# Optimization experiments

Hardware: AMD Instinct MI355X
Metric: run time of the kernel (lower is better)

The kernel has to match this reference:

```python
import jax, jax.numpy as jnp
import numpy as np

B, S, HIDDEN = 2, 2048, 2048
HEADS, GROUPS, KVC = 16, 4, 128
HPG = HEADS // GROUPS  # heads per group
LAYER_INDEX = 2
SOFTMAX_SCALE = KVC ** -0.5
ROPE_THETA = 10000.0


def _rope_tables(seq_len, dim, dtype=jnp.float32):
    inv_freq = 1.0 / (ROPE_THETA ** (jnp.arange(0, dim, 2, dtype=jnp.float32) / dim))
    t = jnp.arange(seq_len, dtype=jnp.float32)
    freqs = jnp.outer(t, inv_freq)  # [S, dim/2]
    return jnp.cos(freqs).astype(dtype), jnp.sin(freqs).astype(dtype)


def _apply_rope(x, cos, sin):
    # x: [b, s, h, d]; rotate-half (GPT-NeoX style)
    d2 = x.shape[-1] // 2
    x1, x2 = x[..., :d2], x[..., d2:]
    c = cos[None, :, None, :]
    s = sin[None, :, None, :]
    return jnp.concatenate([x1 * c - x2 * s, x2 * c + x1 * s], axis=-1)


def setup_inputs() -> dict:
    key = jax.random.key(0)
    k1, k2, k3, k4 = jax.random.split(key, 4)
    std = HIDDEN ** -0.5
    return {
        "x": jax.random.normal(k1, (B, S, HIDDEN), dtype=jnp.float32),
        "w_q": jax.random.normal(k2, (HIDDEN, HEADS * KVC), dtype=jnp.float32) * std,
        "w_kv": jax.random.normal(k3, (HIDDEN, 2 * GROUPS * KVC), dtype=jnp.float32) * std,
        "w_dense": jax.random.normal(k4, (HEADS * KVC, HIDDEN), dtype=jnp.float32) * std,
    }


def reference(x, w_q, w_kv, w_dense):
    b, s, _ = x.shape
    # QKV projections
    q = (x @ w_q).reshape(b, s, HEADS, KVC)                 # [b,s,H,d]
    kv = (x @ w_kv).reshape(b, s, 2, GROUPS, KVC)
    k, v = kv[:, :, 0], kv[:, :, 1]                          # [b,s,G,d]
    # Rotary embeddings on q and k
    cos, sin = _rope_tables(s, KVC, x.dtype)
    q = _apply_rope(q, cos, sin)
    k = _apply_rope(k, cos, sin)
    # GQA attention with per-layer scaling trick:
    # scores computed at scale/softmax of layer_index, cast fp32, rescaled back.
    qg = q.reshape(b, s, GROUPS, HPG, KVC)
    scores = jnp.einsum("bqghd,bkgd->bghqk", qg, k) * (SOFTMAX_SCALE / LAYER_INDEX)
    scores = scores.astype(jnp.float32) * LAYER_INDEX
    # causal mask
    causal = jnp.tril(jnp.ones((s, s), dtype=bool))
    mask_value = jnp.finfo(jnp.float32).min
    scores = jnp.where(causal[None, None, None, :, :], scores, mask_value)
    probs = jax.nn.softmax(scores, axis=-1).astype(x.dtype)  # dropout p=0 (eval)
    ctx = jnp.einsum("bghqk,bkgd->bqghd", probs, v).reshape(b, s, HEADS * KVC)
    return ctx @ w_dense
```

## Files before the change

### kernel.cpp

```cpp
#include <hip/hip_runtime.h>
#include <hip/hip_bf16.h>
#include <stdint.h>

typedef unsigned short u16;
typedef __bf16 bf16x8 __attribute__((ext_vector_type(8)));
typedef float f32x4 __attribute__((ext_vector_type(4)));

#define S_LEN 2048
#define BATCH 2
#define NHEADS 16
#define NGROUPS 4
#define DHEAD 128
#define QKV_W 3072

__device__ __forceinline__ float bf2f(u16 u) {
  union { uint32_t i; float f; } v; v.i = ((uint32_t)u) << 16; return v.f;
}
__device__ __forceinline__ u16 f2bf(float f) {
  union { float f; uint32_t i; } v; v.f = f;
  uint32_t r = v.i + 0x7FFF + ((v.i >> 16) & 1);
  return (u16)(r >> 16);
}
__device__ __forceinline__ void llds16(const void* g, void* l) {
  __builtin_amdgcn_global_load_lds(
      (const __attribute__((address_space(1))) uint32_t*)g,
      (__attribute__((address_space(3))) uint32_t*)l, 16, 0, 0);
}

__device__ __forceinline__ void store_out(u16* C, long i, float v) { C[i] = f2bf(v); }
__device__ __forceinline__ void store_out(float* C, long i, float v) { C[i] = v; }

__global__ void rope_tables_k(float* __restrict__ cosT, float* __restrict__ sinT) {
  int i = blockIdx.x * 256 + threadIdx.x;
  int s = i >> 6, j = i & 63;
  float inv = exp2f(-(float)j * 0.20762050593045983f);
  float ang = (float)s * inv;
  float sv, cv;
  sincosf(ang, &sv, &cv);
  cosT[i] = cv; sinT[i] = sv;
}

__global__ void cvt_f32_bf16(const float* __restrict__ in, u16* __restrict__ out) {
  long i = ((long)blockIdx.x * 256 + threadIdx.x) * 4;
  float4 v = *(const float4*)(in + i);
  ushort4 o;
  o.x = f2bf(v.x); o.y = f2bf(v.y); o.z = f2bf(v.z); o.w = f2bf(v.w);
  *(ushort4*)(out + i) = o;
}

__global__ void transpose_f32_bf16(const float* __restrict__ in, u16* __restrict__ out,
                                   int R, int C) {
  __shared__ u16 tile[32][33];
  int c0 = blockIdx.x * 32, r0 = blockIdx.y * 32;
  int tx = threadIdx.x, ty = threadIdx.y;
  for (int i = 0; i < 32; i += 8)
    tile[ty + i][tx] = f2bf(in[(long)(r0 + ty + i) * C + c0 + tx]);
  __syncthreads();
  for (int i = 0; i < 32; i += 8)
    out[(long)(c0 + ty + i) * R + r0 + tx] = tile[tx][ty + i];
}

#define GFENCE() asm volatile("" ::: "memory")
#define MIDBAR() do { GFENCE(); __builtin_amdgcn_s_barrier(); \
    asm volatile("s_waitcnt lgkmcnt(0)" ::: "memory"); } while (0)
#define ENDBAR() do { GFENCE(); __builtin_amdgcn_s_barrier(); GFENCE(); } while (0)

__device__ __forceinline__ bf16x8 frag_ld(const __bf16* h, int wrow, int kk, int quad) {
  int b = ((wrow & 15) << 6) | (quad << 4);
  b ^= ((wrow >> 3) & 1) << 5;
  int off = ((((wrow >> 4) << 1) | kk) << 10) | b;
  return *(const bf16x8*)((const char*)h + off);
}

__device__ __forceinline__ void stage_half(const u16* __restrict__ g, int K,
                                           __bf16* lhalf, int wv, int lane) {
  int bsrc = (lane << 4) ^ (((lane >> 5) & 1) << 5);
  int r = bsrc >> 6, c = (bsrc & 63) >> 1;
  int cb = (wv & 1) << 5;
  llds16(g + (long)((wv >> 1) * 16 + r) * K + cb + c,
         lhalf + wv * 512 + lane * 8);
  llds16(g + (long)((4 + (wv >> 1)) * 16 + r) * K + cb + c,
         lhalf + 4096 + wv * 512 + lane * 8);
}

template <typename OutT>
__global__ __launch_bounds__(512) void gemm_bt8(
    const u16* __restrict__ A, const u16* __restrict__ Bt, OutT* __restrict__ C,
    int M, int N, int K) {
  __shared__ __align__(16) __bf16 lds[2][2][16384];
  const int tid = threadIdx.x;
  const int wv = tid >> 6, lane = tid & 63;
  const int quad = lane >> 4, l16 = lane & 15;
  const int wr = wv >> 2, wc = wv & 3;

  const int nwg = gridDim.x * gridDim.y;
  const int orig = blockIdx.y * gridDim.x + blockIdx.x;
  const int swz = (orig & 7) * (nwg >> 3) + (orig >> 3);
  const int bx = swz % gridDim.x, by = swz / gridDim.x;
  const int bm = by * 256, bn = bx * 256;

  const u16* Abase = A + (long)bm * K;
  const u16* Bbase = Bt + (long)bn * K;
  const int NT = K >> 6;

  f32x4 acc[8][4] = {};

  stage_half(Abase, K, &lds[0][0][0], wv, lane);
  stage_half(Abase + (long)128 * K, K, &lds[0][0][8192], wv, lane);
  stage_half(Bbase, K, &lds[0][1][0], wv, lane);
  stage_half(Bbase + (long)128 * K, K, &lds[0][1][8192], wv, lane);
  stage_half(Abase + 64, K, &lds[1][0][0], wv, lane);
  stage_half(Abase + (long)128 * K + 64, K, &lds[1][0][8192], wv, lane);
  stage_half(Bbase + 64, K, &lds[1][1][0], wv, lane);
  stage_half(Bbase + (long)128 * K + 64, K, &lds[1][1][8192], wv, lane);
  asm volatile("s_waitcnt vmcnt(8)" ::: "memory");
  __builtin_amdgcn_s_barrier();
  GFENCE();

  for (int kt = 0; kt < NT; ++kt) {
    const int buf = kt & 1;
    const __bf16* Ah = &lds[buf][0][wr * 8192];
    const __bf16* Bh = &lds[buf][1][(wc >> 1) * 8192];
    const int brow0 = (wc & 1) << 6;
    const bool pre = (kt + 2 < NT);
    bf16x8 aF[4][2], bF[4][2];

#pragma unroll
    for (int m = 0; m < 4; ++m) {
      aF[m][0] = frag_ld(Ah, m * 16 + l16, 0, quad);
      aF[m][1] = frag_ld(Ah, m * 16 + l16, 1, quad);
    }
#pragma unroll
    for (int n = 0; n < 2; ++n) {
      bF[n][0] = frag_ld(Bh, brow0 + n * 16 + l16, 0, quad);
      bF[n][1] = frag_ld(Bh, brow0 + n * 16 + l16, 1, quad);
    }
    MIDBAR();
    __builtin_amdgcn_s_setprio(1);
#pragma unroll
    for (int m = 0; m < 4; ++m)
#pragma unroll
      for (int n = 0; n < 2; ++n) {
        acc[m][n] = __builtin_amdgcn_mfma_f32_16x16x32_bf16(aF[m][0], bF[n][0], acc[m][n], 0, 0, 0);
        acc[m][n] = __builtin_amdgcn_mfma_f32_16x16x32_bf16(aF[m][1], bF[n][1], acc[m][n], 0, 0, 0);
      }
    __builtin_amdgcn_s_setprio(0);
    ENDBAR();

#pragma unroll
    for (int n = 2; n < 4; ++n) {
      bF[n][0] = frag_ld(Bh, brow0 + n * 16 + l16, 0, quad);
      bF[n][1] = frag_ld(Bh, brow0 + n * 16 + l16, 1, quad);
    }
    MIDBAR();
    __builtin_amdgcn_s_setprio(1);
#pragma unroll
    for (int m = 0; m < 4; ++m)
#pragma unroll
      for (int n = 2; n < 4; ++n) {
        acc[m][n] = __builtin_amdgcn_mfma_f32_16x16x32_bf16(aF[m][0], bF[n][0], acc[m][n], 0, 0, 0);
        acc[m][n] = __builtin_amdgcn_mfma_f32_16x16x32_bf16(aF[m][1], bF[n][1], acc[m][n], 0, 0, 0);
      }
    __builtin_amdgcn_s_setprio(0);
    ENDBAR();

#pragma unroll
    for (int m = 0; m < 4; ++m) {
      aF[m][0] = frag_ld(Ah, 64 + m * 16 + l16, 0, quad);
      aF[m][1] = frag_ld(Ah, 64 + m * 16 + l16, 1, quad);
    }
    if (pre) {
      const u16* p = Bbase + (long)(kt + 2) * 64;
      stage_half(p, K, &lds[buf][1][0], wv, lane);
      stage_half(p + (long)128 * K, K, &lds[buf][1][8192], wv, lane);
    }
    MIDBAR();
    __builtin_amdgcn_s_setprio(1);
#pragma unroll
    for (int m = 0; m < 4; ++m)
#pragma unroll
      for (int n = 2; n < 4; ++n) {
        acc[4 + m][n] = __builtin_amdgcn_mfma_f32_16x16x32_bf16(aF[m][0], bF[n][0], acc[4 + m][n], 0, 0, 0);
        acc[4 + m][n] = __builtin_amdgcn_mfma_f32_16x16x32_bf16(aF[m][1], bF[n][1], acc[4 + m][n], 0, 0, 0);
      }
    __builtin_amdgcn_s_setprio(0);
    ENDBAR();

    if (pre) {
      const u16* p = Abase + (long)(kt + 2) * 64;
      stage_half(p, K, &lds[buf][0][0], wv, lane);
      stage_half(p + (long)128 * K, K, &lds[buf][0][8192], wv, lane);
    }
    MIDBAR();
    __builtin_amdgcn_s_setprio(1);
#pragma unroll
    for (int m = 0; m < 4; ++m)
#pragma unroll
      for (int n = 0; n < 2; ++n) {
        acc[4 + m][n] = __builtin_amdgcn_mfma_f32_16x16x32_bf16(aF[m][0], bF[n][0], acc[4 + m][n], 0, 0, 0);
        acc[4 + m][n] = __builtin_amdgcn_mfma_f32_16x16x32_bf16(aF[m][1], bF[n][1], acc[4 + m][n], 0, 0, 0);
      }
    __builtin_amdgcn_s_setprio(0);
    if (pre) { asm volatile("s_waitcnt vmcnt(8)" ::: "memory"); }
    else     { asm volatile("s_waitcnt vmcnt(0)" ::: "memory"); }
    ENDBAR();
  }

  const long colbase = (long)bn + wc * 64 + l16;
#pragma unroll
  for (int mt = 0; mt < 8; ++mt)
#pragma unroll
    for (int nt = 0; nt < 4; ++nt)
#pragma unroll
      for (int rr = 0; rr < 4; ++rr) {
        long row = bm + wr * 128 + mt * 16 + quad * 4 + rr;
        store_out(C, row * N + colbase + nt * 16, acc[mt][nt][rr]);
      }
}

__global__ void rope_q_k(u16* __restrict__ qkv, const float* __restrict__ cosT,
                         const float* __restrict__ sinT) {
  long i = (long)blockIdx.x * 256 + threadIdx.x;
  int j = i & 63;
  long rest = i >> 6;
  int h = rest & 15;
  long bs = rest >> 4;
  int s = bs & (S_LEN - 1);
  long base = bs * QKV_W + h * DHEAD + j;
  float x1 = bf2f(qkv[base]), x2 = bf2f(qkv[base + 64]);
  float c = cosT[s * 64 + j], sn = sinT[s * 64 + j];
  qkv[base] = f2bf(x1 * c - x2 * sn);
  qkv[base + 64] = f2bf(x2 * c + x1 * sn);
}

__global__ void rope_k_k(const u16* __restrict__ qkv, u16* __restrict__ Kb,
                         const float* __restrict__ cosT, const float* __restrict__ sinT) {
  long i = (long)blockIdx.x * 256 + threadIdx.x;
  int j = i & 63;
  long rest = i >> 6;
  int g = rest & 3;
  long bs = rest >> 2;
  int s = bs & (S_LEN - 1);
  int b = (int)(bs >> 11);
  long src = bs * QKV_W + 2048 + g * 128 + j;
  float x1 = bf2f(qkv[src]), x2 = bf2f(qkv[src + 64]);
  float c = cosT[s * 64 + j], sn = sinT[s * 64 + j];
  long dst = ((long)(b * NGROUPS + g) * S_LEN + s) * DHEAD + j;
  Kb[dst] = f2bf(x1 * c - x2 * sn);
  Kb[dst + 64] = f2bf(x2 * c + x1 * sn);
}

__global__ void v_trans_k(const u16* __restrict__ qkv, u16* __restrict__ Vt) {
  __shared__ u16 tile[32][33];
  int s0 = blockIdx.x * 32, d0 = blockIdx.y * 32;
  int bg = blockIdx.z;
  int b = bg >> 2, g = bg & 3;
  int tx = threadIdx.x, ty = threadIdx.y;
  for (int i = 0; i < 32; i += 8) {
    long s = s0 + ty + i;
    tile[ty + i][tx] = qkv[((long)b * S_LEN + s) * QKV_W + 2560 + g * 128 + d0 + tx];
  }
  __syncthreads();
  for (int i = 0; i < 32; i += 8) {
    int d = d0 + ty + i;
    Vt[((long)(b * NGROUPS + g) * DHEAD + d) * S_LEN + s0 + tx] = tile[tx][ty + i];
  }
}

__global__ __launch_bounds__(512, 2) void attn_k9(
    const u16* __restrict__ Q,
    const u16* __restrict__ Kb,
    const u16* __restrict__ Vt,
    u16* __restrict__ ctx) {
  __shared__ __align__(16) char smem[82432];
  __bf16* Ks   = (__bf16*)smem;
  __bf16* Vts  = (__bf16*)(smem + 32768);
  __bf16* Ps   = (__bf16*)(smem + 65536);
  float*  Psum = (float*)(smem + 81920);
  float*  scr  = (float*)smem;

  const int h = blockIdx.y, b = blockIdx.z, g = h >> 2;
  const int tx = blockIdx.x;
  const int tid = threadIdx.x, wv = tid >> 6, lane = tid & 63;
  const int quad = lane >> 4, l16 = lane & 15;
  const int rg = wv & 3;
  const int kh = wv >> 2;
  const float SCALE = 0.08838834764831845f;

  const long kbase = (long)(b * NGROUPS + g) * S_LEN * DHEAD;
  const long vbase = (long)(b * NGROUPS + g) * DHEAD * S_LEN;

  const int krow_off = lane >> 4;
  const int vrow_off = lane >> 3;

  const __bf16 oneb = (__bf16)((l16 == 0) ? 1.0f : 0.0f);
  const bf16x8 bones = {oneb, oneb, oneb, oneb, oneb, oneb, oneb, oneb};

  __bf16* Pw = Ps + wv * 1024;

  for (int pass = 0; pass < 2; ++pass) {
    const int tile = pass ? (15 - tx) : tx;
    const int q0 = tile * 128;
    const int nch = 2 * (tile + 1);

    bf16x8 aq[2][4];
#pragma unroll
    for (int m = 0; m < 2; ++m) {
      const u16* qp = Q + (long)(b * S_LEN + q0 + rg * 32 + m * 16 + l16) * QKV_W + h * DHEAD + quad * 8;
#pragma unroll
      for (int ds = 0; ds < 4; ++ds)
        aq[m][ds] = *(const bf16x8*)(qp + ds * 32);
    }

#pragma unroll
    for (int i = 0; i < 2; ++i) {
      int r0 = wv * 8 + i * 4;
      int row = r0 + krow_off;
      int c = l16 ^ (row & 15);
      llds16(Kb + kbase + (long)row * DHEAD + c * 8, &Ks[r0 * 128 + lane * 8]);
    }
#pragma unroll
    for (int i = 0; i < 2; ++i) {
      int d0 = wv * 16 + i * 8;
      int row = d0 + vrow_off;
      int c = (lane & 7) ^ (row & 7);
      llds16(Vt + vbase + (long)row * S_LEN + c * 8, &Vts[d0 * 64 + lane * 8]);
    }
    __syncthreads();

    f32x4 Oacc[2][8] = {};
    f32x4 Osum[2] = {};
    const int rmin = q0 + rg * 32;

    for (int kc = 0; kc < nch; ++kc) {
      const int cur = kc & 1;
      if (kc + 1 < nch) {
        const int nxt = cur ^ 1;
#pragma unroll
        for (int i = 0; i < 2; ++i) {
          int r0 = wv * 8 + i * 4;
          int row = r0 + krow_off;
          int c = l16 ^ (row & 15);
          llds16(Kb + kbase + (long)((kc + 1) * 64 + row) * DHEAD + c * 8,
                 &Ks[nxt * 8192 + r0 * 128 + lane * 8]);
        }
#pragma unroll
        for (int i = 0; i < 2; ++i) {
          int d0 = wv * 16 + i * 8;
          int row = d0 + vrow_off;
          int c = (lane & 7) ^ (row & 7);
          llds16(Vt + vbase + (long)row * S_LEN + (kc + 1) * 64 + c * 8,
                 &Vts[nxt * 8192 + d0 * 64 + lane * 8]);
        }
      }

      const int kb0 = kc * 64 + kh * 32;
      const bool skip = kb0 > (rmin + 31);
      if (!skip) {
        f32x4 sacc[2][2] = {};
        __builtin_amdgcn_s_setprio(1);
#pragma unroll
        for (int ds = 0; ds < 4; ++ds) {
          int pos0 = ((ds * 4 + quad) ^ l16) * 8;
#pragma unroll
          for (int nt = 0; nt < 2; ++nt) {
            bf16x8 bk = *(const bf16x8*)&Ks[cur * 8192 + (kh * 32 + nt * 16 + l16) * 128 + pos0];
            sacc[0][nt] = __builtin_amdgcn_mfma_f32_16x16x32_bf16(aq[0][ds], bk, sacc[0][nt], 0, 0, 0);
            sacc[1][nt] = __builtin_amdgcn_mfma_f32_16x16x32_bf16(aq[1][ds], bk, sacc[1][nt], 0, 0, 0);
          }
        }
        __builtin_amdgcn_s_setprio(0);

        const bool need_mask = (kb0 + 31) > rmin;
        if (need_mask) {
#pragma unroll
          for (int m = 0; m < 2; ++m)
#pragma unroll
            for (int nt = 0; nt < 2; ++nt)
#pragma unroll
              for (int r = 0; r < 4; ++r) {
                int qrow = rmin + m * 16 + quad * 4 + r;
                int key = kb0 + nt * 16 + l16;
                float p = (key <= qrow) ? __expf(sacc[m][nt][r] * SCALE) : 0.f;
                int row = m * 16 + quad * 4 + r;
                int gs = (nt * 2 + (l16 >> 3)) ^ quad;
                Pw[row * 32 + gs * 8 + (l16 & 7)] = (__bf16)p;
              }
        } else {
#pragma unroll
          for (int m = 0; m < 2; ++m)
#pragma unroll
            for (int nt = 0; nt < 2; ++nt)
#pragma unroll
              for (int r = 0; r < 4; ++r) {
                float p = __expf(sacc[m][nt][r] * SCALE);
                int row = m * 16 + quad * 4 + r;
                int gs = (nt * 2 + (l16 >> 3)) ^ quad;
                Pw[row * 32 + gs * 8 + (l16 & 7)] = (__bf16)p;
              }
        }

        bf16x8 ap[2];
#pragma unroll
        for (int m = 0; m < 2; ++m) {
          int pos = (quad ^ ((l16 >> 2) & 3)) * 8;
          ap[m] = *(const bf16x8*)&Pw[(m * 16 + l16) * 32 + pos];
        }
        __builtin_amdgcn_s_setprio(1);
#pragma unroll
        for (int nt = 0; nt < 8; ++nt) {
          int pos = (((kh << 2) | quad) ^ (l16 & 7)) * 8;
          bf16x8 bv = *(const bf16x8*)&Vts[cur * 8192 + (nt * 16 + l16) * 64 + pos];
          Oacc[0][nt] = __builtin_amdgcn_mfma_f32_16x16x32_bf16(ap[0], bv, Oacc[0][nt], 0, 0, 0);
          Oacc[1][nt] = __builtin_amdgcn_mfma_f32_16x16x32_bf16(ap[1], bv, Oacc[1][nt], 0, 0, 0);
        }
#pragma unroll
        for (int m = 0; m < 2; ++m)
          Osum[m] = __builtin_amdgcn_mfma_f32_16x16x32_bf16(ap[m], bones, Osum[m], 0, 0, 0);
        __builtin_amdgcn_s_setprio(0);
      }

      __syncthreads();
    }

    if (kh == 1) {
      float* s = scr + rg * 4096;
#pragma unroll
      for (int m = 0; m < 2; ++m)
#pragma unroll
        for (int nt = 0; nt < 8; ++nt)
#pragma unroll
          for (int r = 0; r < 4; ++r)
            s[(m * 16 + quad * 4 + r) * 128 + nt * 16 + l16] = Oacc[m][nt][r];
      if (l16 == 0) {
#pragma unroll
        for (int m = 0; m < 2; ++m)
#pragma unroll
          for (int r = 0; r < 4; ++r)
            Psum[rg * 32 + m * 16 + quad * 4 + r] = Osum[m][r];
      }
    }
    __syncthreads();
    if (kh == 0) {
      float* s = scr + rg * 4096;
#pragma unroll
      for (int m = 0; m < 2; ++m) {
        float lsum[4];
#pragma unroll
        for (int r = 0; r < 4; ++r)
          lsum[r] = __shfl(Osum[m][r], quad << 4, 64) +
                    Psum[rg * 32 + m * 16 + quad * 4 + r];
        const long obase = ((long)(b * S_LEN + q0 + rg * 32 + m * 16) * NHEADS + h) * DHEAD;
#pragma unroll
        for (int nt = 0; nt < 8; ++nt)
#pragma unroll
          for (int r = 0; r < 4; ++r) {
            int lrow = quad * 4 + r;
            float v = Oacc[m][nt][r] + s[(m * 16 + lrow) * 128 + nt * 16 + l16];
            ctx[obase + (long)lrow * NHEADS * DHEAD + nt * 16 + l16] = f2bf(v / lsum[r]);
          }
      }
    }
    __syncthreads();
  }
}

extern "C" void kernel_launch(void* const* d_in, const int* in_sizes, int n_in,
                              void* d_out, int out_size, void* d_ws, size_t ws_size,
                              hipStream_t stream) {
  const float* x   = (const float*)d_in[0];
  const float* wq  = (const float*)d_in[1];
  const float* wkv = (const float*)d_in[2];
  const float* wd  = (const float*)d_in[3];
  float* out = (float*)d_out;

  char* ws = (char*)d_ws;
  float* cosT  = (float*)(ws + 0);
  float* sinT  = (float*)(ws + 524288);
  u16* wqkvT = (u16*)(ws + 1048576);
  u16* wdT   = (u16*)(ws + 13631488);
  u16* xb    = (u16*)(ws + 22020096);
  u16* qkv   = (u16*)(ws + 38797312);
  u16* Kb    = (u16*)(ws + 63963136);
  u16* Vt    = (u16*)(ws + 68157440);
  u16* ctx   = (u16*)(ws + 72351744);

  rope_tables_k<<<512, 256, 0, stream>>>(cosT, sinT);
  cvt_f32_bf16<<<8192, 256, 0, stream>>>(x, xb);
  transpose_f32_bf16<<<dim3(64, 64), dim3(32, 8), 0, stream>>>(wq, wqkvT, 2048, 2048);
  transpose_f32_bf16<<<dim3(32, 64), dim3(32, 8), 0, stream>>>(wkv, wqkvT + (long)2048 * 2048, 2048, 1024);
  transpose_f32_bf16<<<dim3(64, 64), dim3(32, 8), 0, stream>>>(wd, wdT, 2048, 2048);

  gemm_bt8<u16><<<dim3(12, 16), 512, 0, stream>>>(xb, wqkvT, qkv, 4096, 3072, 2048);

  rope_q_k<<<16384, 256, 0, stream>>>(qkv, cosT, sinT);
  rope_k_k<<<4096, 256, 0, stream>>>(qkv, Kb, cosT, sinT);
  v_trans_k<<<dim3(64, 4, 8), dim3(32, 8), 0, stream>>>(qkv, Vt);

  attn_k9<<<dim3(8, 16, 2), 512, 0, stream>>>(qkv, Kb, Vt, ctx);

  gemm_bt8<float><<<dim3(8, 16), 512, 0, stream>>>(ctx, wdT, out, 4096, 2048, 2048);
}
```

Measured before the change: 316.8 us.

## Fuse Q rotary embedding into attention load and retile output GEMM

Drops the standalone rope_q_k kernel. Rotary embedding is now applied to Q fragments inside the attention kernel as they are loaded, reading the cos/sin tables there, which removes a full read-modify-write pass over Q. Separately, the output projection uses a new GEMM variant with 256x128 tiles (a 16x16 grid instead of 8x16) and fp32 output, to raise workgroup count and improve occupancy. Rounding changes slightly because Q is rotated from bf16 inside the kernel, and the smaller N tile means more A-tile reloads.

```diff
diff --git a/kernel.cpp b/kernel.cpp
--- a/kernel.cpp
+++ b/kernel.cpp
@@ -218,19 +218,104 @@
       }
 }
 
-__global__ void rope_q_k(u16* __restrict__ qkv, const float* __restrict__ cosT,
-                         const float* __restrict__ sinT) {
-  long i = (long)blockIdx.x * 256 + threadIdx.x;
-  int j = i & 63;
-  long rest = i >> 6;
-  int h = rest & 15;
-  long bs = rest >> 4;
-  int s = bs & (S_LEN - 1);
-  long base = bs * QKV_W + h * DHEAD + j;
-  float x1 = bf2f(qkv[base]), x2 = bf2f(qkv[base + 64]);
-  float c = cosT[s * 64 + j], sn = sinT[s * 64 + j];
-  qkv[base] = f2bf(x1 * c - x2 * sn);
-  qkv[base + 64] = f2bf(x2 * c + x1 * sn);
+__global__ __launch_bounds__(512) void gemm_bt8n(
+    const u16* __restrict__ A, const u16* __restrict__ Bt, float* __restrict__ C,
+    int M, int N, int K) {
+  __shared__ __align__(16) __bf16 Abuf[2][16384];
+  __shared__ __align__(16) __bf16 Bbuf[2][8192];
+  const int tid = threadIdx.x;
+  const int wv = tid >> 6, lane = tid & 63;
+  const int quad = lane >> 4, l16 = lane & 15;
+  const int wr = wv >> 2, wc = wv & 3;
+
+  const int nwg = gridDim.x * gridDim.y;
+  const int orig = blockIdx.y * gridDim.x + blockIdx.x;
+  const int swz = (orig & 7) * (nwg >> 3) + (orig >> 3);
+  const int bx = swz % gridDim.x, by = swz / gridDim.x;
+  const int bm = by * 256, bn = bx * 128;
+
+  const u16* Abase = A + (long)bm * K;
+  const u16* Bbase = Bt + (long)bn * K;
+  const int NT = K >> 6;
+
+  f32x4 acc[8][2] = {};
+
+  stage_half(Abase, K, &Abuf[0][0], wv, lane);
+  stage_half(Abase + (long)128 * K, K, &Abuf[0][8192], wv, lane);
+  stage_half(Bbase, K, &Bbuf[0][0], wv, lane);
+  stage_half(Abase + 64, K, &Abuf[1][0], wv, lane);
+  stage_half(Abase + (long)128 * K + 64, K, &Abuf[1][8192], wv, lane);
+  stage_half(Bbase + 64, K, &Bbuf[1][0], wv, lane);
+  asm volatile("s_waitcnt vmcnt(0)" ::: "memory");
+  __builtin_amdgcn_s_barrier();
+  GFENCE();
+
+  for (int kt = 0; kt < NT; ++kt) {
+    const int buf = kt & 1;
+    const __bf16* Ah = &Abuf[buf][wr * 8192];
+    const __bf16* Bh = &Bbuf[buf][0];
+    bf16x8 aF[4][2], bF[2][2];
+
+#pragma unroll
+    for (int m = 0; m < 4; ++m) {
+      aF[m][0] = frag_ld(Ah, m * 16 + l16, 0, quad);
+      aF[m][1] = frag_ld(Ah, m * 16 + l16, 1, quad);
+    }
+#pragma unroll
+    for (int n = 0; n < 2; ++n) {
+      bF[n][0] = frag_ld(Bh, wc * 32 + n * 16 + l16, 0, quad);
+      bF[n][1] = frag_ld(Bh, wc * 32 + n * 16 + l16, 1, quad);
+    }
+    if (kt >= 1 && kt + 1 < NT) {
+      const u16* p = Abase + (long)(kt + 1) * 64;
+      stage_half(p, K, &Abuf[(kt + 1) & 1][0], wv, lane);
+      stage_half(p + (long)128 * K, K, &Abuf[(kt + 1) & 1][8192], wv, lane);
+    }
+    MIDBAR();
+    __builtin_amdgcn_s_setprio(1);
+#pragma unroll
+    for (int m = 0; m < 4; ++m)
+#pragma unroll
+      for (int n = 0; n < 2; ++n) {
+        acc[m][n] = __builtin_amdgcn_mfma_f32_16x16x32_bf16(aF[m][0], bF[n][0], acc[m][n], 0, 0, 0);
+        acc[m][n] = __builtin_amdgcn_mfma_f32_16x16x32_bf16(aF[m][1], bF[n][1], acc[m][n], 0, 0, 0);
+      }
+    __builtin_amdgcn_s_setprio(0);
+    ENDBAR();
+
+#pragma unroll
+    for (int m = 0; m < 4; ++m) {
+      aF[m][0] = frag_ld(Ah, 64 + m * 16 + l16, 0, quad);
+      aF[m][1] = frag_ld(Ah, 64 + m * 16 + l16, 1, quad);
+    }
+    if (kt + 2 < NT) {
+      stage_half(Bbase + (long)(kt + 2) * 64, K, &Bbuf[buf][0], wv, lane);
+    }
+    MIDBAR();
+    __builtin_amdgcn_s_setprio(1);
+#pragma unroll
+    for (int m = 0; m < 4; ++m)
+#pragma unroll
+      for (int n = 0; n < 2; ++n) {
+        acc[4 + m][n] = __builtin_amdgcn_mfma_f32_16x16x32_bf16(aF[m][0], bF[n][0], acc[4 + m][n], 0, 0, 0);
+        acc[4 + m][n] = __builtin_amdgcn_mfma_f32_16x16x32_bf16(aF[m][1], bF[n][1], acc[4 + m][n], 0, 0, 0);
+      }
+    __builtin_amdgcn_s_setprio(0);
+    if (kt + 2 < NT) { asm volatile("s_waitcnt vmcnt(2)" ::: "memory"); }
+    else             { asm volatile("s_waitcnt vmcnt(0)" ::: "memory"); }
+    ENDBAR();
+  }
+
+  const long colbase = (long)bn + wc * 32 + l16;
+#pragma unroll
+  for (int mt = 0; mt < 8; ++mt)
+#pragma unroll
+    for (int nt = 0; nt < 2; ++nt)
+#pragma unroll
+      for (int rr = 0; rr < 4; ++rr) {
+        long row = bm + wr * 128 + mt * 16 + quad * 4 + rr;
+        C[row * N + colbase + nt * 16] = acc[mt][nt][rr];
+      }
 }
 
 __global__ void rope_k_k(const u16* __restrict__ qkv, u16* __restrict__ Kb,
@@ -267,10 +352,11 @@
   }
 }
 
-__global__ __launch_bounds__(512, 2) void attn_k9(
+__global__ __launch_bounds__(512, 2) void attn_k10(
     const u16* __restrict__ Q,
     const u16* __restrict__ Kb,
     const u16* __restrict__ Vt,
+    const float* __restrict__ cosT, const float* __restrict__ sinT,
     u16* __restrict__ ctx) {
   __shared__ __align__(16) char smem[82432];
   __bf16* Ks   = (__bf16*)smem;
@@ -306,10 +392,23 @@
     bf16x8 aq[2][4];
 #pragma unroll
     for (int m = 0; m < 2; ++m) {
-      const u16* qp = Q + (long)(b * S_LEN + q0 + rg * 32 + m * 16 + l16) * QKV_W + h * DHEAD + quad * 8;
+      const int srow = q0 + rg * 32 + m * 16 + l16;
+      const u16* qp = Q + (long)(b * S_LEN + srow) * QKV_W + h * DHEAD + quad * 8;
+      bf16x8 raw[4];
 #pragma unroll
       for (int ds = 0; ds < 4; ++ds)
-        aq[m][ds] = *(const bf16x8*)(qp + ds * 32);
+        raw[ds] = *(const bf16x8*)(qp + ds * 32);
+      const float* cb = cosT + srow * 64 + quad * 8;
+      const float* sb = sinT + srow * 64 + quad * 8;
+#pragma unroll
+      for (int ds = 0; ds < 2; ++ds)
+#pragma unroll
+        for (int e = 0; e < 8; ++e) {
+          float c = cb[ds * 32 + e], s = sb[ds * 32 + e];
+          float lo = (float)raw[ds][e], hi = (float)raw[ds + 2][e];
+          aq[m][ds][e]     = (__bf16)(lo * c - hi * s);
+          aq[m][ds + 2][e] = (__bf16)(hi * c + lo * s);
+        }
     }
 
 #pragma unroll
@@ -493,11 +592,10 @@
 
   gemm_bt8<u16><<<dim3(12, 16), 512, 0, stream>>>(xb, wqkvT, qkv, 4096, 3072, 2048);
 
-  rope_q_k<<<16384, 256, 0, stream>>>(qkv, cosT, sinT);
   rope_k_k<<<4096, 256, 0, stream>>>(qkv, Kb, cosT, sinT);
   v_trans_k<<<dim3(64, 4, 8), dim3(32, 8), 0, stream>>>(qkv, Vt);
 
-  attn_k9<<<dim3(8, 16, 2), 512, 0, stream>>>(qkv, Kb, Vt, ctx);
-
-  gemm_bt8<float><<<dim3(8, 16), 512, 0, stream>>>(ctx, wdT, out, 4096, 2048, 2048);
-}
+  attn_k10<<<dim3(8, 16, 2), 512, 0, stream>>>(qkv, Kb, Vt, cosT, sinT, ctx);
+
+  gemm_bt8n<<<dim3(16, 16), 512, 0, stream>>>(ctx, wdT, out, 4096, 2048, 2048);
+}
```

Result: faster. 290.9 us (-8.2%).
